# Kernel tuning notes

Hardware: AMD Instinct MI355X
Metric: run time of the kernel (lower is better)

The kernel has to match this reference:

```python
import jax, jax.numpy as jnp
import numpy as np

HIDDEN = 768
INTER = 3072
HEADS = 12
HEAD_DIM = INTER // HEADS  # 256
LN_EPS = 1e-6
R_SOFTPLUS_0 = 1.442695041


def setup_inputs() -> dict:
    key = jax.random.key(0)
    ks = jax.random.split(key, 12)
    s = 0.02
    inp = {
        "hidden_states": jax.random.normal(ks[0], (8, 4096, HIDDEN), dtype=jnp.float32),
        "pooling_query": jax.random.normal(ks[1], (1, 1, HIDDEN), dtype=jnp.float32) * s,
        "Wq": jax.random.normal(ks[2], (HIDDEN, INTER), dtype=jnp.float32) * s,
        "bq": jnp.zeros((INTER,), dtype=jnp.float32),
        "Wk": jax.random.normal(ks[3], (HIDDEN, INTER), dtype=jnp.float32) * s,
        "bk": jnp.zeros((INTER,), dtype=jnp.float32),
        "Wv": jax.random.normal(ks[4], (HIDDEN, INTER), dtype=jnp.float32) * s,
        "bv": jnp.zeros((INTER,), dtype=jnp.float32),
        "Wp": jax.random.normal(ks[5], (INTER, HIDDEN), dtype=jnp.float32) * s,
        "bp": jnp.zeros((HIDDEN,), dtype=jnp.float32),
        "per_dim_scale": jnp.zeros((HEAD_DIM,), dtype=jnp.float32),
        "ln_w": jnp.ones((HIDDEN,), dtype=jnp.float32),
        "ln_b": jnp.zeros((HIDDEN,), dtype=jnp.float32),
    }
    return inp


def reference(hidden_states, pooling_query, Wq, bq, Wk, bk, Wv, bv, Wp, bp,
              per_dim_scale, ln_w, ln_b):
    B, S, _ = hidden_states.shape
    dt = hidden_states.dtype

    # Query: single pooling token, identical across batch -> [H, D]
    q = (pooling_query.reshape(1, HIDDEN) @ Wq + bq).reshape(HEADS, HEAD_DIM)
    # PerDimScale: q * (r_softplus0/sqrt(D)) * softplus(per_dim_scale)
    scale = (R_SOFTPLUS_0 / np.sqrt(HEAD_DIM)).astype(np.float32)
    q = q * (scale * jax.nn.softplus(per_dim_scale))

    # K/V projections: [B, S, H, D]
    k = (hidden_states @ Wk + bk).reshape(B, S, HEADS, HEAD_DIM)
    v = (hidden_states @ Wv + bv).reshape(B, S, HEADS, HEAD_DIM)

    # Single-query attention: logits [B, H, S]; scaling=1.0 (scale_logits_by_head_dims=False)
    # logit cap skipped (no_attention_logit_cap=True)
    logits = jnp.einsum("hd,bshd->bhs", q, k)
    attn = jax.nn.softmax(logits.astype(jnp.float32), axis=-1).astype(dt)

    # Weighted sum over seq: [B, H, D] -> concat heads -> [B, H*D]
    ctx = jnp.einsum("bhs,bshd->bhd", attn, v).reshape(B, HEADS * HEAD_DIM)

    out = ctx @ Wp + bp  # [B, HIDDEN]
    # LayerNorm; note the original forward adds ones to ln weight in-place each call,
    # so effective weight for one call is (ln_w + 1).
    mean = jnp.mean(out, axis=-1, keepdims=True)
    var = jnp.var(out, axis=-1, keepdims=True)
    out = (out - mean) * jax.lax.rsqrt(var + LN_EPS) * (ln_w + 1.0) + ln_b

    pooled = out[:, None, :]  # [B, 1, HIDDEN]
    attn_weights = attn[:, :, None, :]  # [B, H, 1, S]
    return pooled, attn_weights
```

## Files before the change

kernel.cpp:

```cpp
#include <hip/hip_runtime.h>
#include <cstdint>
#include <cmath>

#define LN_EPS 1e-6f

#define N_QCH 24u
#define O_QPART 0u
#define O_Q     73728u
#define O_WK    76800u
#define O_PLOG  86016u
#define O_PHP   1658880u
#define N_SC    32
#define O_CTXP  4091904u
#define N_CCH   12
#define O_OUTP  4411392u
#define N_ICH   48
#define O_ATT   4706304u

__device__ __forceinline__ float waveReduceSum(float v) {
#pragma unroll
    for (int o = 32; o >= 1; o >>= 1) v += __shfl_xor(v, o, 64);
    return v;
}
__device__ __forceinline__ float waveReduceMax(float v) {
#pragma unroll
    for (int o = 32; o >= 1; o >>= 1) v = fmaxf(v, __shfl_xor(v, o, 64));
    return v;
}

__global__ __launch_bounds__(256) void k1_qpart(const float* __restrict__ pq,
                                                const float* __restrict__ Wq,
                                                float* __restrict__ ws) {
    int h = blockIdx.x % 12;
    int ch = blockIdx.x / 12;
    int tid = threadIdx.x;
    int col = h * 256 + tid;
    int c0 = ch * 32;
    float acc = 0.f;
#pragma unroll 8
    for (int i = 0; i < 32; ++i) {
        int c = c0 + i;
        acc += pq[c] * Wq[c * 3072 + col];
    }
    ws[O_QPART + ch * 3072 + col] = acc;
}

__global__ __launch_bounds__(256) void k1b_qreduce(const float* __restrict__ bq,
                                                   const float* __restrict__ pds,
                                                   float* __restrict__ ws) {
    int j = blockIdx.x * 256 + threadIdx.x;
    float acc = bq[j];
#pragma unroll
    for (unsigned ch = 0; ch < N_QCH; ++ch) acc += ws[O_QPART + ch * 3072 + j];
    float x = pds[j & 255];
    float sp = (x > 20.f) ? x : log1pf(expf(x));
    const float scale = 1.442695041f / 16.0f;
    ws[O_Q + j] = acc * scale * sp;
}

__global__ __launch_bounds__(256) void k2_wkeff(const float* __restrict__ Wk,
                                                float* __restrict__ ws) {
    int c = blockIdx.x;
    int tid = threadIdx.x;
    int w = tid >> 6, lane = tid & 63;
    const float4* wk = reinterpret_cast<const float4*>(Wk + (size_t)c * 3072);
    const float4* qv = reinterpret_cast<const float4*>(ws + O_Q);
#pragma unroll
    for (int i = 0; i < 3; ++i) {
        int h = w * 3 + i;
        float4 a = wk[h * 64 + lane];
        float4 b = qv[h * 64 + lane];
        float d = a.x * b.x + a.y * b.y + a.z * b.z + a.w * b.w;
        d = waveReduceSum(d);
        if (lane == 0) ws[O_WK + c * 12 + h] = d;
    }
}

__global__ __launch_bounds__(256) void k3_logits(const float* __restrict__ hidden,
                                                 const float* __restrict__ wk,
                                                 float* __restrict__ plog) {
    __shared__ float4 tile4[2][768];
    int blk = blockIdx.x;
    int q = blk & 3;
    int st = (blk >> 2) & 63;
    int b = blk >> 8;
    int s0 = st * 64;
    const float* hb = hidden + (size_t)(b * 4096 + s0) * 768 + q * 192;
    int tid = threadIdx.x;
    int w = tid >> 6, lane = tid & 63;
    int rr[3], jj[3];
#pragma unroll
    for (int t = 0; t < 3; ++t) {
        int idx = t * 256 + tid;
        rr[t] = idx / 12;
        jj[t] = idx % 12;
    }
    float4 v[3];
#pragma unroll
    for (int t = 0; t < 3; ++t)
        v[t] = *reinterpret_cast<const float4*>(hb + rr[t] * 768 + jj[t] * 4);

    float acc[12];
#pragma unroll
    for (int h = 0; h < 12; ++h) acc[h] = 0.f;

    for (int ck = 0; ck < 4; ++ck) {
        float4* buf = tile4[ck & 1];
#pragma unroll
        for (int t = 0; t < 3; ++t)
            buf[rr[t] * 12 + (jj[t] ^ (rr[t] & 3))] = v[t];
        if (ck < 3) {
#pragma unroll
            for (int t = 0; t < 3; ++t)
                v[t] = *reinterpret_cast<const float4*>(hb + rr[t] * 768 + (ck + 1) * 48 + jj[t] * 4);
        }
        int wkoff = __builtin_amdgcn_readfirstlane((q * 192 + ck * 48 + (tid >> 6) * 12) * 12);
        const float* wr = wk + wkoff;
        __syncthreads();
#pragma unroll
        for (int j2 = 0; j2 < 3; ++j2) {
            int jcol = w * 3 + j2;
            float4 x = buf[lane * 12 + (jcol ^ (lane & 3))];
            const float* wv = wr + j2 * 48;
            float xc[4] = {x.x, x.y, x.z, x.w};
#pragma unroll
            for (int cc = 0; cc < 4; ++cc) {
                const float* wc = wv + cc * 12;
#pragma unroll
                for (int h = 0; h < 12; ++h)
                    acc[h] += xc[cc] * wc[h];
            }
        }
    }
    float* red = reinterpret_cast<float*>(tile4);
#pragma unroll
    for (int h = 0; h < 12; ++h) red[(w * 12 + h) * 64 + lane] = acc[h];
    __syncthreads();
    for (int idx = tid; idx < 768; idx += 256) {
        int h = idx / 64, r2 = idx & 63;
        float vv = red[(0 + h) * 64 + r2] + red[(12 + h) * 64 + r2] +
                   red[(24 + h) * 64 + r2] + red[(36 + h) * 64 + r2];
        plog[(size_t)q * 393216 + (size_t)(b * 12 + h) * 4096 + s0 + r2] = vv;
    }
}

__global__ __launch_bounds__(256) void k4_softmax(const float* __restrict__ ws,
                                                  float* __restrict__ attn,
                                                  float* __restrict__ attn_t) {
    __shared__ float sh[4];
    int row = blockIdx.x;
    const float4* p0 = reinterpret_cast<const float4*>(ws + O_PLOG + (size_t)row * 4096);
    const float4* p1 = p0 + 98304;
    const float4* p2 = p0 + 196608;
    const float4* p3 = p0 + 294912;
    float* base = attn + (size_t)row * 4096;
    int b = row / 12, h = row % 12;
    float* at = attn_t + (size_t)b * 65536 + h;
    int tid = threadIdx.x;
    float4 x[4];
#pragma unroll
    for (int t = 0; t < 4; ++t) {
        float4 a = p0[t * 256 + tid], c = p1[t * 256 + tid];
        float4 d = p2[t * 256 + tid], e = p3[t * 256 + tid];
        x[t].x = (a.x + c.x) + (d.x + e.x);
        x[t].y = (a.y + c.y) + (d.y + e.y);
        x[t].z = (a.z + c.z) + (d.z + e.z);
        x[t].w = (a.w + c.w) + (d.w + e.w);
    }
    float m = -1e30f;
#pragma unroll
    for (int t = 0; t < 4; ++t)
        m = fmaxf(m, fmaxf(fmaxf(x[t].x, x[t].y), fmaxf(x[t].z, x[t].w)));
    m = waveReduceMax(m);
    if ((tid & 63) == 0) sh[tid >> 6] = m;
    __syncthreads();
    m = fmaxf(fmaxf(sh[0], sh[1]), fmaxf(sh[2], sh[3]));
    __syncthreads();
    float s = 0.f;
#pragma unroll
    for (int t = 0; t < 4; ++t) {
        x[t].x = expf(x[t].x - m); x[t].y = expf(x[t].y - m);
        x[t].z = expf(x[t].z - m); x[t].w = expf(x[t].w - m);
        s += x[t].x + x[t].y + x[t].z + x[t].w;
    }
    s = waveReduceSum(s);
    if ((tid & 63) == 0) sh[tid >> 6] = s;
    __syncthreads();
    s = sh[0] + sh[1] + sh[2] + sh[3];
    float inv = 1.0f / s;
#pragma unroll
    for (int t = 0; t < 4; ++t) {
        x[t].x *= inv; x[t].y *= inv; x[t].z *= inv; x[t].w *= inv;
        reinterpret_cast<float4*>(base)[t * 256 + tid] = x[t];
        int sb = (t * 256 + tid) * 4;
        at[(size_t)(sb + 0) * 16] = x[t].x;
        at[(size_t)(sb + 1) * 16] = x[t].y;
        at[(size_t)(sb + 2) * 16] = x[t].z;
        at[(size_t)(sb + 3) * 16] = x[t].w;
    }
}

__global__ __launch_bounds__(256) void k5_phpart(const float* __restrict__ hidden,
                                                 const float* __restrict__ attn_t,
                                                 float* __restrict__ php) {
    __shared__ float4 sh4[6 * 4 * 64];
    int blk = blockIdx.x;
    int sc = blk & 31;
    int ct = (blk >> 5) % 3;
    int b = blk / 96;
    int tid = threadIdx.x;
    int w = tid >> 6, lane = tid & 63;
    int c = ct * 256 + lane * 4;
    int s0 = sc * 128 + w * 32;
    const float* hb = hidden + (size_t)(b * 4096 + s0) * 768 + c;
    float4 acc[12];
#pragma unroll
    for (int h = 0; h < 12; ++h) acc[h] = make_float4(0.f, 0.f, 0.f, 0.f);
#pragma unroll 4
    for (int g = 0; g < 32; ++g) {
        float4 x = *reinterpret_cast<const float4*>(hb + (size_t)g * 768);
        int aoff = __builtin_amdgcn_readfirstlane((b * 4096 + sc * 128 + (tid >> 6) * 32 + g) * 16);
        const float* ar = attn_t + aoff;
        float a[12];
#pragma unroll
        for (int h = 0; h < 12; ++h) a[h] = ar[h];
#pragma unroll
        for (int h = 0; h < 12; ++h) {
            acc[h].x += a[h] * x.x; acc[h].y += a[h] * x.y;
            acc[h].z += a[h] * x.z; acc[h].w += a[h] * x.w;
        }
    }
    float* phpb = php + (size_t)(sc * 96 + b * 12) * 768 + ct * 256;
#pragma unroll
    for (int r = 0; r < 2; ++r) {
        if (r) __syncthreads();
#pragma unroll
        for (int i = 0; i < 6; ++i)
            sh4[(i * 4 + w) * 64 + lane] = acc[r * 6 + i];
        __syncthreads();
#pragma unroll
        for (int t = 0; t < 2; ++t) {
            int idx = t * 256 + tid;
            if (idx < 384) {
                int i = idx >> 6, l = idx & 63;
                float4 A = sh4[(i * 4 + 0) * 64 + l];
                float4 B = sh4[(i * 4 + 1) * 64 + l];
                float4 C = sh4[(i * 4 + 2) * 64 + l];
                float4 D = sh4[(i * 4 + 3) * 64 + l];
                float4 r4;
                r4.x = (A.x + B.x) + (C.x + D.x);
                r4.y = (A.y + B.y) + (C.y + D.y);
                r4.z = (A.z + B.z) + (C.z + D.z);
                r4.w = (A.w + B.w) + (C.w + D.w);
                *reinterpret_cast<float4*>(phpb + (size_t)(r * 6 + i) * 768 + l * 4) = r4;
            }
        }
    }
}

__global__ __launch_bounds__(256) void k7_ctxpart(const float* __restrict__ Wv,
                                                  float* __restrict__ ws) {
    __shared__ float phl[512];
    int blk = blockIdx.x;
    int jt = blk % 12, cch = blk / 12;
    int tid = threadIdx.x;
    const float* php = ws + O_PHP;
#pragma unroll
    for (int t = 0; t < 2; ++t) {
        int idx = t * 256 + tid;
        int b = idx >> 6, cc = idx & 63;
        int c = cch * 64 + cc;
        const float* p = php + (size_t)(b * 12 + jt) * 768 + c;
        float s = 0.f;
#pragma unroll
        for (int sc = 0; sc < N_SC; ++sc) s += p[(size_t)sc * 73728];
        phl[idx] = s;
    }
    __syncthreads();
    int j = jt * 256 + tid;
    float acc[8];
#pragma unroll
    for (int b = 0; b < 8; ++b) acc[b] = 0.f;
    for (int cc = 0; cc < 64; ++cc) {
        int c = cch * 64 + cc;
        float wv = Wv[(size_t)c * 3072 + j];
#pragma unroll
        for (int b = 0; b < 8; ++b) acc[b] += phl[b * 64 + cc] * wv;
    }
#pragma unroll
    for (int b = 0; b < 8; ++b)
        ws[O_CTXP + (size_t)(cch * 8 + b) * 3072 + j] = acc[b];
}

__global__ __launch_bounds__(256) void k8_outpart(const float* __restrict__ Wp,
                                                  const float* __restrict__ bv,
                                                  float* __restrict__ ws) {
    __shared__ float ctxl[512];
    int blk = blockIdx.x;
    int jt = blk % 3, ich = blk / 3;
    int tid = threadIdx.x;
#pragma unroll
    for (int t = 0; t < 2; ++t) {
        int idx = t * 256 + tid;
        int b = idx >> 6, ii = idx & 63;
        int i = ich * 64 + ii;
        float s = bv[i];
#pragma unroll
        for (int cch = 0; cch < N_CCH; ++cch)
            s += ws[O_CTXP + (size_t)(cch * 8 + b) * 3072 + i];
        ctxl[idx] = s;
    }
    __syncthreads();
    int j = jt * 256 + tid;
    float acc[8];
#pragma unroll
    for (int b = 0; b < 8; ++b) acc[b] = 0.f;
    for (int ii = 0; ii < 64; ++ii) {
        int i = ich * 64 + ii;
        float wp = Wp[(size_t)i * 768 + j];
#pragma unroll
        for (int b = 0; b < 8; ++b) acc[b] += ctxl[b * 64 + ii] * wp;
    }
#pragma unroll
    for (int b = 0; b < 8; ++b)
        ws[O_OUTP + (size_t)(ich * 8 + b) * 768 + j] = acc[b];
}

__global__ __launch_bounds__(256) void k9_ln(const float* __restrict__ bp,
                                             const float* __restrict__ ln_w,
                                             const float* __restrict__ ln_b,
                                             const float* __restrict__ ws,
                                             float* __restrict__ pooled) {
    __shared__ float sh[8];
    int b = blockIdx.x, tid = threadIdx.x;
    const float* op = ws + O_OUTP;
    float vals[3];
    float lsum = 0.f, lsq = 0.f;
#pragma unroll
    for (int t = 0; t < 3; ++t) {
        int j = t * 256 + tid;
        float v = bp[j];
#pragma unroll
        for (int ich = 0; ich < N_ICH; ++ich) v += op[(size_t)(ich * 8 + b) * 768 + j];
        vals[t] = v; lsum += v; lsq += v * v;
    }
    lsum = waveReduceSum(lsum);
    lsq = waveReduceSum(lsq);
    if ((tid & 63) == 0) { sh[tid >> 6] = lsum; sh[4 + (tid >> 6)] = lsq; }
    __syncthreads();
    float mean = (sh[0] + sh[1] + sh[2] + sh[3]) * (1.f / 768.f);
    float var = (sh[4] + sh[5] + sh[6] + sh[7]) * (1.f / 768.f) - mean * mean;
    float inv = rsqrtf(var + LN_EPS);
#pragma unroll
    for (int t = 0; t < 3; ++t) {
        int j = t * 256 + tid;
        pooled[b * 768 + j] = (vals[t] - mean) * inv * (ln_w[j] + 1.f) + ln_b[j];
    }
}

extern "C" void kernel_launch(void* const* d_in, const int* in_sizes, int n_in,
                              void* d_out, int out_size, void* d_ws, size_t ws_size,
                              hipStream_t stream) {
    const float* hidden = (const float*)d_in[0];
    const float* pq     = (const float*)d_in[1];
    const float* Wq     = (const float*)d_in[2];
    const float* bq     = (const float*)d_in[3];
    const float* Wk     = (const float*)d_in[4];
    const float* Wv     = (const float*)d_in[6];
    const float* bv     = (const float*)d_in[7];
    const float* Wp     = (const float*)d_in[8];
    const float* bp     = (const float*)d_in[9];
    const float* pds    = (const float*)d_in[10];
    const float* ln_w   = (const float*)d_in[11];
    const float* ln_b   = (const float*)d_in[12];
    float* out = (float*)d_out;
    float* ws  = (float*)d_ws;
    float* pooled = out;
    float* attn   = out + 6144;

    k1_qpart   <<<288, 256, 0, stream>>>(pq, Wq, ws);
    k1b_qreduce<<<12, 256, 0, stream>>>(bq, pds, ws);
    k2_wkeff   <<<768, 256, 0, stream>>>(Wk, ws);
    k3_logits  <<<2048, 256, 0, stream>>>(hidden, ws + O_WK, ws + O_PLOG);
    k4_softmax <<<96, 256, 0, stream>>>(ws, attn, ws + O_ATT);
    k5_phpart  <<<768, 256, 0, stream>>>(hidden, ws + O_ATT, ws + O_PHP);
    k7_ctxpart <<<144, 256, 0, stream>>>(Wv, ws);
    k8_outpart <<<144, 256, 0, stream>>>(Wp, bv, ws);
    k9_ln      <<<8, 256, 0, stream>>>(bp, ln_w, ln_b, ws, pooled);
}
```

Before: 268.3 us.

## Fuse query projection kernels and halve logits column split with double-buffered loads

Merges the two query-projection kernels into one 48-block kernel that reduces its four row-group partials in shared memory, removing a launch and a workspace round trip. The logits kernel now splits the hidden dimension into 2 chunks instead of 4, so it launches half as many blocks. Each block prefetches two tiles ahead through explicitly unrolled double buffers and uses a lighter LDS-only barrier. The softmax kernel accordingly sums 2 partial-logit planes instead of 4. The cost is less parallelism in the logits kernel and a serial 192-step loop per thread in the query kernel.

```diff
diff --git a/kernel.cpp b/kernel.cpp
--- a/kernel.cpp
+++ b/kernel.cpp
@@ -4,8 +4,6 @@
 
 #define LN_EPS 1e-6f
 
-#define N_QCH 24u
-#define O_QPART 0u
 #define O_Q     73728u
 #define O_WK    76800u
 #define O_PLOG  86016u
@@ -28,34 +26,38 @@
     return v;
 }
 
-__global__ __launch_bounds__(256) void k1_qpart(const float* __restrict__ pq,
-                                                const float* __restrict__ Wq,
-                                                float* __restrict__ ws) {
-    int h = blockIdx.x % 12;
-    int ch = blockIdx.x / 12;
-    int tid = threadIdx.x;
-    int col = h * 256 + tid;
-    int c0 = ch * 32;
+__device__ __forceinline__ void block_sync_lds() {
+    asm volatile("s_waitcnt lgkmcnt(0)" ::: "memory");
+    __builtin_amdgcn_s_barrier();
+    asm volatile("" ::: "memory");
+}
+
+__global__ __launch_bounds__(256) void k1_q(const float* __restrict__ pq,
+                                            const float* __restrict__ Wq,
+                                            const float* __restrict__ bq,
+                                            const float* __restrict__ pds,
+                                            float* __restrict__ ws) {
+    __shared__ float sh[4][64];
+    int tid = threadIdx.x;
+    int l = tid & 63;
+    int rg = tid >> 6;
+    int col = blockIdx.x * 64 + l;
+    const float* wq = Wq + (size_t)(rg * 192) * 3072 + col;
+    const float* pr = pq + rg * 192;
     float acc = 0.f;
 #pragma unroll 8
-    for (int i = 0; i < 32; ++i) {
-        int c = c0 + i;
-        acc += pq[c] * Wq[c * 3072 + col];
-    }
-    ws[O_QPART + ch * 3072 + col] = acc;
-}
-
-__global__ __launch_bounds__(256) void k1b_qreduce(const float* __restrict__ bq,
-                                                   const float* __restrict__ pds,
-                                                   float* __restrict__ ws) {
-    int j = blockIdx.x * 256 + threadIdx.x;
-    float acc = bq[j];
-#pragma unroll
-    for (unsigned ch = 0; ch < N_QCH; ++ch) acc += ws[O_QPART + ch * 3072 + j];
-    float x = pds[j & 255];
-    float sp = (x > 20.f) ? x : log1pf(expf(x));
-    const float scale = 1.442695041f / 16.0f;
-    ws[O_Q + j] = acc * scale * sp;
+    for (int i = 0; i < 192; ++i)
+        acc += pr[i] * wq[(size_t)i * 3072];
+    sh[rg][l] = acc;
+    __syncthreads();
+    if (tid < 64) {
+        int j = blockIdx.x * 64 + tid;
+        float a = sh[0][tid] + sh[1][tid] + sh[2][tid] + sh[3][tid] + bq[j];
+        float x = pds[j & 255];
+        float sp = (x > 20.f) ? x : log1pf(expf(x));
+        const float scale = 1.442695041f / 16.0f;
+        ws[O_Q + j] = a * scale * sp;
+    }
 }
 
 __global__ __launch_bounds__(256) void k2_wkeff(const float* __restrict__ Wk,
@@ -81,11 +83,11 @@
                                                  float* __restrict__ plog) {
     __shared__ float4 tile4[2][768];
     int blk = blockIdx.x;
-    int q = blk & 3;
-    int st = (blk >> 2) & 63;
-    int b = blk >> 8;
+    int q2 = blk & 1;
+    int st = (blk >> 1) & 63;
+    int b = blk >> 7;
     int s0 = st * 64;
-    const float* hb = hidden + (size_t)(b * 4096 + s0) * 768 + q * 192;
+    const float* hb = hidden + (size_t)(b * 4096 + s0) * 768 + q2 * 384;
     int tid = threadIdx.x;
     int w = tid >> 6, lane = tid & 63;
     int rr[3], jj[3];
@@ -95,28 +97,30 @@
         rr[t] = idx / 12;
         jj[t] = idx % 12;
     }
-    float4 v[3];
+    float4 v0[3], v1[3];
 #pragma unroll
     for (int t = 0; t < 3; ++t)
-        v[t] = *reinterpret_cast<const float4*>(hb + rr[t] * 768 + jj[t] * 4);
+        v0[t] = *reinterpret_cast<const float4*>(hb + rr[t] * 768 + jj[t] * 4);
+#pragma unroll
+    for (int t = 0; t < 3; ++t)
+        v1[t] = *reinterpret_cast<const float4*>(hb + rr[t] * 768 + 48 + jj[t] * 4);
 
     float acc[12];
 #pragma unroll
     for (int h = 0; h < 12; ++h) acc[h] = 0.f;
 
-    for (int ck = 0; ck < 4; ++ck) {
-        float4* buf = tile4[ck & 1];
+    auto step = [&](float4 (&v)[3], float4* buf, int ck) {
 #pragma unroll
         for (int t = 0; t < 3; ++t)
             buf[rr[t] * 12 + (jj[t] ^ (rr[t] & 3))] = v[t];
-        if (ck < 3) {
+        if (ck < 6) {
 #pragma unroll
             for (int t = 0; t < 3; ++t)
-                v[t] = *reinterpret_cast<const float4*>(hb + rr[t] * 768 + (ck + 1) * 48 + jj[t] * 4);
+                v[t] = *reinterpret_cast<const float4*>(hb + rr[t] * 768 + (ck + 2) * 48 + jj[t] * 4);
         }
-        int wkoff = __builtin_amdgcn_readfirstlane((q * 192 + ck * 48 + (tid >> 6) * 12) * 12);
+        int wkoff = __builtin_amdgcn_readfirstlane((q2 * 384 + ck * 48 + (tid >> 6) * 12) * 12);
         const float* wr = wk + wkoff;
-        __syncthreads();
+        block_sync_lds();
 #pragma unroll
         for (int j2 = 0; j2 < 3; ++j2) {
             int jcol = w * 3 + j2;
@@ -131,6 +135,11 @@
                     acc[h] += xc[cc] * wc[h];
             }
         }
+    };
+#pragma unroll
+    for (int ck2 = 0; ck2 < 8; ck2 += 2) {
+        step(v0, tile4[0], ck2);
+        step(v1, tile4[1], ck2 + 1);
     }
     float* red = reinterpret_cast<float*>(tile4);
 #pragma unroll
@@ -140,7 +149,7 @@
         int h = idx / 64, r2 = idx & 63;
         float vv = red[(0 + h) * 64 + r2] + red[(12 + h) * 64 + r2] +
                    red[(24 + h) * 64 + r2] + red[(36 + h) * 64 + r2];
-        plog[(size_t)q * 393216 + (size_t)(b * 12 + h) * 4096 + s0 + r2] = vv;
+        plog[(size_t)q2 * 393216 + (size_t)(b * 12 + h) * 4096 + s0 + r2] = vv;
     }
 }
 
@@ -151,8 +160,6 @@
     int row = blockIdx.x;
     const float4* p0 = reinterpret_cast<const float4*>(ws + O_PLOG + (size_t)row * 4096);
     const float4* p1 = p0 + 98304;
-    const float4* p2 = p0 + 196608;
-    const float4* p3 = p0 + 294912;
     float* base = attn + (size_t)row * 4096;
     int b = row / 12, h = row % 12;
     float* at = attn_t + (size_t)b * 65536 + h;
@@ -161,11 +168,10 @@
 #pragma unroll
     for (int t = 0; t < 4; ++t) {
         float4 a = p0[t * 256 + tid], c = p1[t * 256 + tid];
-        float4 d = p2[t * 256 + tid], e = p3[t * 256 + tid];
-        x[t].x = (a.x + c.x) + (d.x + e.x);
-        x[t].y = (a.y + c.y) + (d.y + e.y);
-        x[t].z = (a.z + c.z) + (d.z + e.z);
-        x[t].w = (a.w + c.w) + (d.w + e.w);
+        x[t].x = a.x + c.x;
+        x[t].y = a.y + c.y;
+        x[t].z = a.z + c.z;
+        x[t].w = a.w + c.w;
     }
     float m = -1e30f;
 #pragma unroll
@@ -378,10 +384,9 @@
     float* pooled = out;
     float* attn   = out + 6144;
 
-    k1_qpart   <<<288, 256, 0, stream>>>(pq, Wq, ws);
-    k1b_qreduce<<<12, 256, 0, stream>>>(bq, pds, ws);
+    k1_q       <<<48, 256, 0, stream>>>(pq, Wq, bq, pds, ws);
     k2_wkeff   <<<768, 256, 0, stream>>>(Wk, ws);
-    k3_logits  <<<2048, 256, 0, stream>>>(hidden, ws + O_WK, ws + O_PLOG);
+    k3_logits  <<<1024, 256, 0, stream>>>(hidden, ws + O_WK, ws + O_PLOG);
     k4_softmax <<<96, 256, 0, stream>>>(ws, attn, ws + O_ATT);
     k5_phpart  <<<768, 256, 0, stream>>>(hidden, ws + O_ATT, ws + O_PHP);
     k7_ctxpart <<<144, 256, 0, stream>>>(Wv, ws);
```

New measurement: 269.5 us. No clear change (+0.5%).
